# Optimization experiments

Hardware: AMD Instinct MI355X
Metric: run time of the kernel (lower is better)

The kernel has to match this reference:

```python
import jax, jax.numpy as jnp
import numpy as np

EPS = 1e-12  # F.normalize default eps

def setup_inputs() -> dict:
    key = jax.random.key(0)
    k1, k2, k3, k4, k5, k6 = jax.random.split(key, 6)
    B, N, F_in, F_out = 8, 2048, 128, 128
    h = jax.random.normal(k1, (B, N, F_in), dtype=jnp.float32)
    # binary adjacency with avg degree ~32 (p = 32/2048)
    adj = (jax.random.uniform(k2, (B, N, N)) < (32.0 / N)).astype(jnp.float32)
    lim = 1.0 / np.sqrt(F_in)
    W_self = jax.random.uniform(k3, (F_in, F_out), minval=-lim, maxval=lim, dtype=jnp.float32)
    b_self = jax.random.uniform(k4, (F_out,), minval=-lim, maxval=lim, dtype=jnp.float32)
    W_neigh = jax.random.uniform(k5, (F_in, F_out), minval=-lim, maxval=lim, dtype=jnp.float32)
    b_neigh = jax.random.uniform(k6, (F_out,), minval=-lim, maxval=lim, dtype=jnp.float32)
    return {"h": h, "adj": adj, "W_self": W_self, "b_self": b_self,
            "W_neigh": W_neigh, "b_neigh": b_neigh}

def reference(h, adj, W_self, b_self, W_neigh, b_neigh):
    # Original builds (B,N,N,F) = adj[:, i, :, None] * h then mean over dim=-2.
    # mean divides by N (not degree), so aggregated = (adj @ h) / N. Fused form:
    N = h.shape[1]
    aggregated = jnp.einsum('bij,bjf->bif', adj, h) / N  # (B,N,F_in)
    out = h @ W_self + b_self + aggregated @ W_neigh + b_neigh
    out = jax.nn.relu(out)
    # F.normalize(p=2, dim=-1): x / max(||x||, eps)
    norm = jnp.linalg.norm(out, axis=-1, keepdims=True)
    out = out / jnp.maximum(norm, EPS)
    return out  # dropout(p=0.0) is identity
```

## Files before the change

### kernel.cpp

```cpp
#include <hip/hip_runtime.h>

typedef unsigned short u16;
typedef unsigned int u32;
typedef unsigned long long u64;

#define BATCH 8
#define NNODE 2048
#define FEAT  128
#define CAP   320

__global__ __launch_bounds__(256) void agg_sparse_kernel(
    const float* __restrict__ adj,
    const float* __restrict__ h,
    float* __restrict__ agg)
{
  __shared__ int sIdx[4][CAP];
  const int tid = threadIdx.x;
  const int l = tid & 63;
  const int w = tid >> 6;
  const int row = blockIdx.x * 4 + w;
  const int b = row >> 11;
  const float* arow = adj + (size_t)row * NNODE;
  const float* hB   = h + (size_t)b * NNODE * FEAT;
  const int l2 = 2 * l;
  int* idx = sIdx[w];

  float4 v[8];
#pragma unroll
  for (int i = 0; i < 8; i++)
    v[i] = *(const float4*)(arow + i * 256 + l * 4);

  float ax = 0.0f, ay = 0.0f;
  int base = 0;

#pragma unroll
  for (int i = 0; i < 8; i++) {
#pragma unroll
    for (int c = 0; c < 4; c++) {
      float a = (c == 0) ? v[i].x : (c == 1) ? v[i].y : (c == 2) ? v[i].z : v[i].w;
      bool nz = (a != 0.0f);
      u64 m = __ballot(nz);
      if (m == 0) continue;
      int pre = __builtin_amdgcn_mbcnt_hi(
          (u32)(m >> 32), __builtin_amdgcn_mbcnt_lo((u32)m, 0));
      int pos = base + pre;
      if (nz && pos < CAP) idx[pos] = i * 256 + 4 * l + c;
      u64 md = __ballot(nz && pos >= CAP);
      while (md) {
        int s = (int)__builtin_ctzll(md);
        md &= md - 1;
        const float2 g = *(const float2*)(hB + (size_t)(i * 256 + 4 * s + c) * FEAT + l2);
        ax += g.x; ay += g.y;
      }
      base += (int)__builtin_popcountll(m);
    }
  }
  const int n = (base < CAP) ? base : CAP;

  int i = 0;
  for (; i + 8 <= n; i += 8) {
    int4 j0 = *(const int4*)&idx[i];
    int4 j1 = *(const int4*)&idx[i + 4];
    float2 g0 = *(const float2*)(hB + (size_t)j0.x * FEAT + l2);
    float2 g1 = *(const float2*)(hB + (size_t)j0.y * FEAT + l2);
    float2 g2 = *(const float2*)(hB + (size_t)j0.z * FEAT + l2);
    float2 g3 = *(const float2*)(hB + (size_t)j0.w * FEAT + l2);
    float2 g4 = *(const float2*)(hB + (size_t)j1.x * FEAT + l2);
    float2 g5 = *(const float2*)(hB + (size_t)j1.y * FEAT + l2);
    float2 g6 = *(const float2*)(hB + (size_t)j1.z * FEAT + l2);
    float2 g7 = *(const float2*)(hB + (size_t)j1.w * FEAT + l2);
    ax += ((g0.x + g1.x) + (g2.x + g3.x)) + ((g4.x + g5.x) + (g6.x + g7.x));
    ay += ((g0.y + g1.y) + (g2.y + g3.y)) + ((g4.y + g5.y) + (g6.y + g7.y));
  }
  for (; i < n; i++) {
    int j = idx[i];
    const float2 g = *(const float2*)(hB + (size_t)j * FEAT + l2);
    ax += g.x; ay += g.y;
  }

  const float invN = 1.0f / (float)NNODE;
  float2 res;
  res.x = ax * invN;
  res.y = ay * invN;
  *(float2*)(agg + (size_t)row * FEAT + l2) = res;
}

#define APITCH 68
#define BPITCH 132

__global__ __launch_bounds__(256) void linear_kernel(
    const float* __restrict__ h,
    const float* __restrict__ agg,
    const float* __restrict__ Ws,
    const float* __restrict__ bs,
    const float* __restrict__ Wn,
    const float* __restrict__ bn,
    float* __restrict__ out)
{
  __shared__ float sA[64 * APITCH];
  __shared__ float sB[64 * BPITCH];

  const int tid = threadIdx.x;
  const int tx = tid & 15;
  const int rg = tid >> 4;
  const int r0 = blockIdx.x * 64;

  float acc[4][8];
#pragma unroll
  for (int r = 0; r < 4; r++)
#pragma unroll
    for (int c = 0; c < 8; c++) acc[r][c] = 0.0f;

  const int arl = tid >> 2;
  const int aq  = tid & 3;
  const int bkl = tid >> 2;
  const int bq  = tid & 3;

  for (int t = 0; t < 4; t++) {
    const float* Asrc = ((t < 2) ? h : agg) + (size_t)(t & 1) * 64;
    const float* Bsrc = (t < 2) ? (Ws + (size_t)(t * 64) * FEAT)
                                : (Wn + (size_t)((t - 2) * 64) * FEAT);
    __syncthreads();
    {
      const float* src = Asrc + (size_t)(r0 + arl) * FEAT + aq * 4;
#pragma unroll
      for (int ii = 0; ii < 4; ii++) {
        float4 vv = *(const float4*)(src + ii * 16);
        int kk = aq * 4 + ii * 16;
        sA[(kk + 0) * APITCH + arl] = vv.x;
        sA[(kk + 1) * APITCH + arl] = vv.y;
        sA[(kk + 2) * APITCH + arl] = vv.z;
        sA[(kk + 3) * APITCH + arl] = vv.w;
      }
    }
    {
      const float* src = Bsrc + (size_t)bkl * FEAT;
#pragma unroll
      for (int j = 0; j < 8; j++) {
        int cw = (bq + 4 * j) * 4;
        *(float4*)&sB[bkl * BPITCH + cw] = *(const float4*)(src + cw);
      }
    }
    __syncthreads();
#pragma unroll 4
    for (int k = 0; k < 64; k++) {
      float4 av = *(const float4*)&sA[k * APITCH + rg * 4];
      float4 b0 = *(const float4*)&sB[k * BPITCH + tx * 8];
      float4 b1 = *(const float4*)&sB[k * BPITCH + tx * 8 + 4];
      const float a[4] = {av.x, av.y, av.z, av.w};
      const float bb[8] = {b0.x, b0.y, b0.z, b0.w, b1.x, b1.y, b1.z, b1.w};
#pragma unroll
      for (int r = 0; r < 4; r++)
#pragma unroll
        for (int c = 0; c < 8; c++)
          acc[r][c] += a[r] * bb[c];
    }
  }

  float4 bsv0 = *(const float4*)(bs + tx * 8);
  float4 bsv1 = *(const float4*)(bs + tx * 8 + 4);
  float4 bnv0 = *(const float4*)(bn + tx * 8);
  float4 bnv1 = *(const float4*)(bn + tx * 8 + 4);
  float bias[8];
  bias[0] = bsv0.x + bnv0.x; bias[1] = bsv0.y + bnv0.y;
  bias[2] = bsv0.z + bnv0.z; bias[3] = bsv0.w + bnv0.w;
  bias[4] = bsv1.x + bnv1.x; bias[5] = bsv1.y + bnv1.y;
  bias[6] = bsv1.z + bnv1.z; bias[7] = bsv1.w + bnv1.w;

  float ss[4] = {0.f, 0.f, 0.f, 0.f};
#pragma unroll
  for (int r = 0; r < 4; r++)
#pragma unroll
    for (int c = 0; c < 8; c++) {
      float vv = acc[r][c] + bias[c];
      if (vv < 0.0f) vv = 0.0f;
      acc[r][c] = vv;
      ss[r] += vv * vv;
    }
#pragma unroll
  for (int r = 0; r < 4; r++) {
    float s = ss[r];
    s += __shfl_xor(s, 1);
    s += __shfl_xor(s, 2);
    s += __shfl_xor(s, 4);
    s += __shfl_xor(s, 8);
    float nrm = sqrtf(s);
    if (nrm < 1e-12f) nrm = 1e-12f;
    ss[r] = 1.0f / nrm;
  }
#pragma unroll
  for (int r = 0; r < 4; r++) {
    float* orow = out + (size_t)(r0 + rg * 4 + r) * FEAT + tx * 8;
    float4 w0, w1;
    w0.x = acc[r][0] * ss[r]; w0.y = acc[r][1] * ss[r];
    w0.z = acc[r][2] * ss[r]; w0.w = acc[r][3] * ss[r];
    w1.x = acc[r][4] * ss[r]; w1.y = acc[r][5] * ss[r];
    w1.z = acc[r][6] * ss[r]; w1.w = acc[r][7] * ss[r];
    *(float4*)(orow) = w0;
    *(float4*)(orow + 4) = w1;
  }
}

extern "C" void kernel_launch(void* const* d_in, const int* in_sizes, int n_in,
                              void* d_out, int out_size, void* d_ws, size_t ws_size,
                              hipStream_t stream) {
  const float* h   = (const float*)d_in[0];
  const float* adj = (const float*)d_in[1];
  const float* Ws  = (const float*)d_in[2];
  const float* bs  = (const float*)d_in[3];
  const float* Wn  = (const float*)d_in[4];
  const float* bn  = (const float*)d_in[5];
  float* out = (float*)d_out;
  float* agg = (float*)d_ws;

  (void)in_sizes; (void)n_in; (void)out_size; (void)ws_size;

  agg_sparse_kernel<<<dim3(BATCH * NNODE / 4), dim3(256), 0, stream>>>(adj, h, agg);
  linear_kernel<<<dim3(BATCH * NNODE / 64), dim3(256), 0, stream>>>(
      h, agg, Ws, bs, Wn, bn, out);
}
```

Baseline: 233.2 us.

## Prefetch next adjacency row per wave and restructure linear kernel tiling

The aggregation kernel now processes 8 rows per wave, loading the next adjacency row into registers while gathering neighbor features for the current row, to hide global load latency. The linear kernel uses 512 threads with 2 rows per thread over the full K=128 in one LDS tile, reading weights directly from global/cache instead of staging them in LDS. The risks are reduced occupancy from the smaller aggregation grid and more global traffic for the weights.

Measured after the change: 272.0 us. 1.17x slower.

```diff
diff --git a/kernel.cpp b/kernel.cpp
--- a/kernel.cpp
+++ b/kernel.cpp
@@ -1,6 +1,5 @@
 #include <hip/hip_runtime.h>
 
-typedef unsigned short u16;
 typedef unsigned int u32;
 typedef unsigned long long u64;
 
@@ -8,6 +7,7 @@
 #define NNODE 2048
 #define FEAT  128
 #define CAP   320
+#define RPW   8
 
 __global__ __launch_bounds__(256) void agg_sparse_kernel(
     const float* __restrict__ adj,
@@ -18,77 +18,93 @@
   const int tid = threadIdx.x;
   const int l = tid & 63;
   const int w = tid >> 6;
-  const int row = blockIdx.x * 4 + w;
-  const int b = row >> 11;
-  const float* arow = adj + (size_t)row * NNODE;
-  const float* hB   = h + (size_t)b * NNODE * FEAT;
+  const int row0 = (blockIdx.x * 4 + w) * RPW;
+  const int b = row0 >> 11;
+  const float* hB = h + (size_t)b * NNODE * FEAT;
   const int l2 = 2 * l;
   int* idx = sIdx[w];
 
-  float4 v[8];
-#pragma unroll
-  for (int i = 0; i < 8; i++)
-    v[i] = *(const float4*)(arow + i * 256 + l * 4);
-
-  float ax = 0.0f, ay = 0.0f;
-  int base = 0;
-
-#pragma unroll
-  for (int i = 0; i < 8; i++) {
-#pragma unroll
-    for (int c = 0; c < 4; c++) {
-      float a = (c == 0) ? v[i].x : (c == 1) ? v[i].y : (c == 2) ? v[i].z : v[i].w;
-      bool nz = (a != 0.0f);
-      u64 m = __ballot(nz);
-      if (m == 0) continue;
-      int pre = __builtin_amdgcn_mbcnt_hi(
-          (u32)(m >> 32), __builtin_amdgcn_mbcnt_lo((u32)m, 0));
-      int pos = base + pre;
-      if (nz && pos < CAP) idx[pos] = i * 256 + 4 * l + c;
-      u64 md = __ballot(nz && pos >= CAP);
-      while (md) {
-        int s = (int)__builtin_ctzll(md);
-        md &= md - 1;
-        const float2 g = *(const float2*)(hB + (size_t)(i * 256 + 4 * s + c) * FEAT + l2);
-        ax += g.x; ay += g.y;
+  float4 vc[8], vn[8];
+  {
+    const float* a0 = adj + (size_t)row0 * NNODE;
+#pragma unroll
+    for (int i = 0; i < 8; i++)
+      vc[i] = *(const float4*)(a0 + i * 256 + l * 4);
+  }
+
+  for (int r = 0; r < RPW; r++) {
+    const int row = row0 + r;
+    if (r + 1 < RPW) {
+      const float* an = adj + (size_t)(row + 1) * NNODE;
+#pragma unroll
+      for (int i = 0; i < 8; i++)
+        vn[i] = *(const float4*)(an + i * 256 + l * 4);
+    }
+
+    float ax = 0.0f, ay = 0.0f;
+    int base = 0;
+#pragma unroll
+    for (int i = 0; i < 8; i++) {
+#pragma unroll
+      for (int c = 0; c < 4; c++) {
+        float a = (c == 0) ? vc[i].x : (c == 1) ? vc[i].y
+                 : (c == 2) ? vc[i].z : vc[i].w;
+        bool nz = (a != 0.0f);
+        u64 m = __ballot(nz);
+        if (m == 0) continue;
+        int pre = __builtin_amdgcn_mbcnt_hi(
+            (u32)(m >> 32), __builtin_amdgcn_mbcnt_lo((u32)m, 0));
+        int pos = base + pre;
+        if (nz && pos < CAP) idx[pos] = i * 256 + 4 * l + c;
+        u64 md = __ballot(nz && pos >= CAP);
+        while (md) {
+          int s = (int)__builtin_ctzll(md);
+          md &= md - 1;
+          const float2 g = *(const float2*)(hB + (size_t)(i * 256 + 4 * s + c) * FEAT + l2);
+          ax += g.x; ay += g.y;
+        }
+        base += (int)__builtin_popcountll(m);
       }
-      base += (int)__builtin_popcountll(m);
-    }
-  }
-  const int n = (base < CAP) ? base : CAP;
-
-  int i = 0;
-  for (; i + 8 <= n; i += 8) {
-    int4 j0 = *(const int4*)&idx[i];
-    int4 j1 = *(const int4*)&idx[i + 4];
-    float2 g0 = *(const float2*)(hB + (size_t)j0.x * FEAT + l2);
-    float2 g1 = *(const float2*)(hB + (size_t)j0.y * FEAT + l2);
-    float2 g2 = *(const float2*)(hB + (size_t)j0.z * FEAT + l2);
-    float2 g3 = *(const float2*)(hB + (size_t)j0.w * FEAT + l2);
-    float2 g4 = *(const float2*)(hB + (size_t)j1.x * FEAT + l2);
-    float2 g5 = *(const float2*)(hB + (size_t)j1.y * FEAT + l2);
-    float2 g6 = *(const float2*)(hB + (size_t)j1.z * FEAT + l2);
-    float2 g7 = *(const float2*)(hB + (size_t)j1.w * FEAT + l2);
-    ax += ((g0.x + g1.x) + (g2.x + g3.x)) + ((g4.x + g5.x) + (g6.x + g7.x));
-    ay += ((g0.y + g1.y) + (g2.y + g3.y)) + ((g4.y + g5.y) + (g6.y + g7.y));
-  }
-  for (; i < n; i++) {
-    int j = idx[i];
-    const float2 g = *(const float2*)(hB + (size_t)j * FEAT + l2);
-    ax += g.x; ay += g.y;
-  }
-
-  const float invN = 1.0f / (float)NNODE;
-  float2 res;
-  res.x = ax * invN;
-  res.y = ay * invN;
-  *(float2*)(agg + (size_t)row * FEAT + l2) = res;
+    }
+    const int n = (base < CAP) ? base : CAP;
+
+    int i = 0;
+    for (; i + 8 <= n; i += 8) {
+      int4 j0 = *(const int4*)&idx[i];
+      int4 j1 = *(const int4*)&idx[i + 4];
+      float2 g0 = *(const float2*)(hB + (size_t)j0.x * FEAT + l2);
+      float2 g1 = *(const float2*)(hB + (size_t)j0.y * FEAT + l2);
+      float2 g2 = *(const float2*)(hB + (size_t)j0.z * FEAT + l2);
+      float2 g3 = *(const float2*)(hB + (size_t)j0.w * FEAT + l2);
+      float2 g4 = *(const float2*)(hB + (size_t)j1.x * FEAT + l2);
+      float2 g5 = *(const float2*)(hB + (size_t)j1.y * FEAT + l2);
+      float2 g6 = *(const float2*)(hB + (size_t)j1.z * FEAT + l2);
+      float2 g7 = *(const float2*)(hB + (size_t)j1.w * FEAT + l2);
+      ax += ((g0.x + g1.x) + (g2.x + g3.x)) + ((g4.x + g5.x) + (g6.x + g7.x));
+      ay += ((g0.y + g1.y) + (g2.y + g3.y)) + ((g4.y + g5.y) + (g6.y + g7.y));
+    }
+    for (; i < n; i++) {
+      int j = idx[i];
+      const float2 g = *(const float2*)(hB + (size_t)j * FEAT + l2);
+      ax += g.x; ay += g.y;
+    }
+
+    const float invN = 1.0f / (float)NNODE;
+    float2 res;
+    res.x = ax * invN;
+    res.y = ay * invN;
+    *(float2*)(agg + (size_t)row * FEAT + l2) = res;
+
+    if (r + 1 < RPW) {
+#pragma unroll
+      for (int i2 = 0; i2 < 8; i2++) vc[i2] = vn[i2];
+    }
+  }
 }
 
 #define APITCH 68
-#define BPITCH 132
-
-__global__ __launch_bounds__(256) void linear_kernel(
+
+__global__ __launch_bounds__(512) void linear_kernel(
     const float* __restrict__ h,
     const float* __restrict__ agg,
     const float* __restrict__ Ws,
@@ -97,63 +113,51 @@
     const float* __restrict__ bn,
     float* __restrict__ out)
 {
-  __shared__ float sA[64 * APITCH];
-  __shared__ float sB[64 * BPITCH];
+  __shared__ float sA[128 * APITCH];
 
   const int tid = threadIdx.x;
   const int tx = tid & 15;
   const int rg = tid >> 4;
   const int r0 = blockIdx.x * 64;
 
-  float acc[4][8];
-#pragma unroll
-  for (int r = 0; r < 4; r++)
+  float acc[2][8];
+#pragma unroll
+  for (int r = 0; r < 2; r++)
 #pragma unroll
     for (int c = 0; c < 8; c++) acc[r][c] = 0.0f;
 
-  const int arl = tid >> 2;
-  const int aq  = tid & 3;
-  const int bkl = tid >> 2;
-  const int bq  = tid & 3;
-
-  for (int t = 0; t < 4; t++) {
-    const float* Asrc = ((t < 2) ? h : agg) + (size_t)(t & 1) * 64;
-    const float* Bsrc = (t < 2) ? (Ws + (size_t)(t * 64) * FEAT)
-                                : (Wn + (size_t)((t - 2) * 64) * FEAT);
+  const int arl = tid >> 3;
+  const int aq  = tid & 7;
+
+  for (int t = 0; t < 2; t++) {
+    const float* Asrc = (t == 0) ? h : agg;
+    const float* Bsrc = (t == 0) ? Ws : Wn;
     __syncthreads();
     {
       const float* src = Asrc + (size_t)(r0 + arl) * FEAT + aq * 4;
 #pragma unroll
-      for (int ii = 0; ii < 4; ii++) {
-        float4 vv = *(const float4*)(src + ii * 16);
-        int kk = aq * 4 + ii * 16;
+      for (int i = 0; i < 4; i++) {
+        float4 vv = *(const float4*)(src + i * 32);
+        int kk = aq * 4 + i * 32;
         sA[(kk + 0) * APITCH + arl] = vv.x;
         sA[(kk + 1) * APITCH + arl] = vv.y;
         sA[(kk + 2) * APITCH + arl] = vv.z;
         sA[(kk + 3) * APITCH + arl] = vv.w;
       }
     }
-    {
-      const float* src = Bsrc + (size_t)bkl * FEAT;
-#pragma unroll
-      for (int j = 0; j < 8; j++) {
-        int cw = (bq + 4 * j) * 4;
-        *(float4*)&sB[bkl * BPITCH + cw] = *(const float4*)(src + cw);
+    __syncthreads();
+#pragma unroll 8
+    for (int k = 0; k < 128; k++) {
+      const float* bp = Bsrc + (size_t)k * FEAT + tx * 8;
+      float4 b0 = *(const float4*)(bp);
+      float4 b1 = *(const float4*)(bp + 4);
+      float2 av = *(const float2*)&sA[k * APITCH + rg * 2];
+      const float bb[8] = {b0.x, b0.y, b0.z, b0.w, b1.x, b1.y, b1.z, b1.w};
+#pragma unroll
+      for (int c = 0; c < 8; c++) {
+        acc[0][c] += av.x * bb[c];
+        acc[1][c] += av.y * bb[c];
       }
-    }
-    __syncthreads();
-#pragma unroll 4
-    for (int k = 0; k < 64; k++) {
-      float4 av = *(const float4*)&sA[k * APITCH + rg * 4];
-      float4 b0 = *(const float4*)&sB[k * BPITCH + tx * 8];
-      float4 b1 = *(const float4*)&sB[k * BPITCH + tx * 8 + 4];
-      const float a[4] = {av.x, av.y, av.z, av.w};
-      const float bb[8] = {b0.x, b0.y, b0.z, b0.w, b1.x, b1.y, b1.z, b1.w};
-#pragma unroll
-      for (int r = 0; r < 4; r++)
-#pragma unroll
-        for (int c = 0; c < 8; c++)
-          acc[r][c] += a[r] * bb[c];
     }
   }
 
@@ -167,9 +171,9 @@
   bias[4] = bsv1.x + bnv1.x; bias[5] = bsv1.y + bnv1.y;
   bias[6] = bsv1.z + bnv1.z; bias[7] = bsv1.w + bnv1.w;
 
-  float ss[4] = {0.f, 0.f, 0.f, 0.f};
-#pragma unroll
-  for (int r = 0; r < 4; r++)
+  float ss[2] = {0.f, 0.f};
+#pragma unroll
+  for (int r = 0; r < 2; r++)
 #pragma unroll
     for (int c = 0; c < 8; c++) {
       float vv = acc[r][c] + bias[c];
@@ -178,7 +182,7 @@
       ss[r] += vv * vv;
     }
 #pragma unroll
-  for (int r = 0; r < 4; r++) {
+  for (int r = 0; r < 2; r++) {
     float s = ss[r];
     s += __shfl_xor(s, 1);
     s += __shfl_xor(s, 2);
@@ -189,8 +193,8 @@
     ss[r] = 1.0f / nrm;
   }
 #pragma unroll
-  for (int r = 0; r < 4; r++) {
-    float* orow = out + (size_t)(r0 + rg * 4 + r) * FEAT + tx * 8;
+  for (int r = 0; r < 2; r++) {
+    float* orow = out + (size_t)(r0 + rg * 2 + r) * FEAT + tx * 8;
     float4 w0, w1;
     w0.x = acc[r][0] * ss[r]; w0.y = acc[r][1] * ss[r];
     w0.z = acc[r][2] * ss[r]; w0.w = acc[r][3] * ss[r];
@@ -215,7 +219,7 @@
 
   (void)in_sizes; (void)n_in; (void)out_size; (void)ws_size;
 
-  agg_sparse_kernel<<<dim3(BATCH * NNODE / 4), dim3(256), 0, stream>>>(adj, h, agg);
-  linear_kernel<<<dim3(BATCH * NNODE / 64), dim3(256), 0, stream>>>(
+  agg_sparse_kernel<<<dim3(BATCH * NNODE / (4 * RPW)), dim3(256), 0, stream>>>(adj, h, agg);
+  linear_kernel<<<dim3(BATCH * NNODE / 64), dim3(512), 0, stream>>>(
       h, agg, Ws, bs, Wn, bn, out);
 }
```
